# Kernel optimization log

Hardware: AMD Instinct MI355X
Metric: run time of the kernel (lower is better)

## Reference

```python
import jax, jax.numpy as jnp
import numpy as np

B, DIM, T = 8, 1024, 4096
CB, CD = 4096, 8          # codebook_size, codebook_dim
COMMIT = 0.25
EPS = 1e-12


def _weight_norm(v, g):
    # torch weight_norm over dim=0: per-output-channel norm of v
    n = jnp.sqrt(jnp.sum(v * v, axis=1, keepdims=True))
    return g[:, None] * v / n


def _l2_normalize(x):
    n = jnp.sqrt(jnp.sum(x * x, axis=1, keepdims=True))
    return x / jnp.maximum(n, EPS)


def setup_inputs() -> dict:
    key = jax.random.key(0)
    ks = jax.random.split(key, 5)
    z = jax.random.normal(ks[0], (B, DIM, T), jnp.float32)
    v_in = jax.random.normal(ks[1], (CD, DIM), jnp.float32) * 0.02   # conv1d k=1 weight (squeezed)
    g_in = jnp.sqrt(jnp.sum(v_in * v_in, axis=1))                     # weight_norm init: g = ||v||
    b_in = jnp.zeros((CD,), jnp.float32)
    codebook = jax.random.normal(ks[2], (CB, CD), jnp.float32)        # nn.Embedding default N(0,1)
    v_out = jax.random.normal(ks[3], (DIM, CD), jnp.float32) * 0.02
    g_out = jnp.sqrt(jnp.sum(v_out * v_out, axis=1))
    b_out = jnp.zeros((DIM,), jnp.float32)
    return {"z": z, "v_in": v_in, "g_in": g_in, "b_in": b_in,
            "codebook": codebook, "v_out": v_out, "g_out": g_out, "b_out": b_out}


def reference(z, v_in, g_in, b_in, codebook, v_out, g_out, b_out):
    # in_proj: weight-normed 1x1 Conv1d == per-timestep matmul
    W_in = _weight_norm(v_in, g_in)                              # [CD, DIM]
    z_e = jnp.einsum('od,bdt->bot', W_in, z) + b_in[None, :, None]  # [B, CD, T]

    # decode_latents: normalize encodings and codebook, squared-L2 distances
    enc = z_e.transpose(0, 2, 1).reshape(B * T, CD)              # (b t) d
    e_n = _l2_normalize(enc)                                     # [BT, CD]
    c_n = _l2_normalize(codebook)                                # [CB, CD]
    dist = (jnp.sum(e_n * e_n, axis=1, keepdims=True)
            - 2.0 * (e_n @ c_n.T)
            + jnp.sum(c_n * c_n, axis=1)[None, :])               # [BT, CB]
    indices = jnp.argmin(dist, axis=1).reshape(B, T)             # [B, T] int

    # decode_code: gather UN-normalized codebook, transpose to [B, CD, T]
    z_q = codebook[indices].transpose(0, 2, 1)                   # [B, CD, T]

    # training losses (per-batch), commitment + codebook
    sg = jax.lax.stop_gradient
    commitment_loss = jnp.mean((z_e - sg(z_q)) ** 2, axis=(1, 2)) * COMMIT
    codebook_loss = jnp.mean((z_q - sg(z_e)) ** 2, axis=(1, 2))
    commit_loss = commitment_loss + codebook_loss                # [B]

    # straight-through estimator
    z_q_ste = z_e + sg(z_q - z_e)                                # [B, CD, T]

    # out_proj
    W_out = _weight_norm(v_out, g_out)                           # [DIM, CD]
    out = jnp.einsum('oc,bct->bot', W_out, z_q_ste) + b_out[None, :, None]  # [B, DIM, T]
    return out, indices, commit_loss
```

## Files before the change

### kernel.cpp

```cpp
#include <hip/hip_runtime.h>

#define DIMN 1024
#define TN 4096
#define BN 8
#define CBN 4096
#define CDN 8
#define BTN (BN*TN)
#define OUT_ELEMS (BN*DIMN*TN)

typedef float fx4 __attribute__((ext_vector_type(4)));

#define WS_WINT 0
#define WS_WOUT 8192
#define WS_CN   16384
#define WS_C2   49152
#define WS_LOSS 86016
#define WS_CNT  86024
#define WS_ZEP  360448

#define LCB_F   0
#define LH_F    32768
#define LZE_F   36864
#define LEN_F   37888
#define LCAND_F 38912
#define LWO_F   0
#define LZQ_F   8192
#define LBO_F   9216

__device__ __forceinline__ float dot4(float4 a, float4 b) {
    float d = a.x * b.x;
    d = fmaf(a.y, b.y, d);
    d = fmaf(a.z, b.z, d);
    d = fmaf(a.w, b.w, d);
    return d;
}
__device__ __forceinline__ void add4(float4& a, float4 b) {
    a.x += b.x; a.y += b.y; a.z += b.z; a.w += b.w;
}

__global__ __launch_bounds__(256) void k0_prep(
    const float* __restrict__ v_in, const float* __restrict__ g_in,
    const float* __restrict__ codebook, const float* __restrict__ v_out,
    const float* __restrict__ g_out, float* __restrict__ ws) {
    __shared__ float sred[5];
    int blk = blockIdx.x, tid = threadIdx.x;
    if (blk < 8) {
        int o = blk;
        const float* v = v_in + o * DIMN;
        float4 x = *(const float4*)(v + tid * 4);
        float p = x.x * x.x + x.y * x.y + x.z * x.z + x.w * x.w;
        for (int off = 32; off >= 1; off >>= 1) p += __shfl_down(p, off, 64);
        if ((tid & 63) == 0) sred[tid >> 6] = p;
        __syncthreads();
        if (tid == 0) {
            float tot = sred[0] + sred[1] + sred[2] + sred[3];
            sred[4] = g_in[o] / sqrtf(tot);
        }
        __syncthreads();
        float s = sred[4];
        ws[WS_WINT + (tid * 4 + 0) * 8 + o] = x.x * s;
        ws[WS_WINT + (tid * 4 + 1) * 8 + o] = x.y * s;
        ws[WS_WINT + (tid * 4 + 2) * 8 + o] = x.z * s;
        ws[WS_WINT + (tid * 4 + 3) * 8 + o] = x.w * s;
    } else if (blk < 12) {
        int r = (blk - 8) * 256 + tid;
        const float* v = v_out + r * 8;
        float4 a = *(const float4*)v;
        float4 b = *(const float4*)(v + 4);
        float n2 = dot4(a, a) + dot4(b, b);
        float s = g_out[r] / sqrtf(n2);
        *(float4*)(ws + WS_WOUT + r * 8)     = make_float4(a.x*s, a.y*s, a.z*s, a.w*s);
        *(float4*)(ws + WS_WOUT + r * 8 + 4) = make_float4(b.x*s, b.y*s, b.z*s, b.w*s);
    } else if (blk < 28) {
        int j = (blk - 12) * 256 + tid;
        const float* c = codebook + j * 8;
        float4 a = *(const float4*)c;
        float4 b = *(const float4*)(c + 4);
        float n2 = dot4(a, a) + dot4(b, b);
        float inv = 1.0f / fmaxf(sqrtf(n2), 1e-12f);
        float4 na = make_float4(a.x*inv, a.y*inv, a.z*inv, a.w*inv);
        float4 nb = make_float4(b.x*inv, b.y*inv, b.z*inv, b.w*inv);
        *(float4*)(ws + WS_CN + j * 8)     = na;
        *(float4*)(ws + WS_CN + j * 8 + 4) = nb;
        ws[WS_C2 + j] = -0.5f * (dot4(na, na) + dot4(nb, nb));
    } else {
        if (tid < 9) ws[WS_LOSS + tid] = 0.0f;
    }
}

__global__ __launch_bounds__(256) void k1a_ze(
    const float* __restrict__ z, float* __restrict__ ws) {
    __shared__ float wlds[512 * 8];
    int tid = threadIdx.x, blk = blockIdx.x;
    int b = blk >> 5;
    int r = blk & 31;
    int t0 = (r >> 1) * 256;
    int dbase = (r & 1) * 512;
    #pragma unroll
    for (int i = 0; i < 4; i++) {
        int f4 = tid + i * 256;
        *(float4*)(wlds + f4 * 4) = *(const float4*)(ws + WS_WINT + dbase * 8 + f4 * 4);
    }
    __syncthreads();
    int w = tid >> 6, lane = tid & 63;
    const float* zp = z + ((size_t)(b * DIMN + dbase + w * 128)) * TN + t0 + lane * 4;
    float4 acc[8];
    #pragma unroll
    for (int c = 0; c < 8; c++) acc[c] = make_float4(0.f, 0.f, 0.f, 0.f);
    #pragma unroll 8
    for (int dd = 0; dd < 128; ++dd) {
        fx4 zr = __builtin_nontemporal_load((const fx4*)(zp + (size_t)dd * TN));
        const float* wv = wlds + (w * 128 + dd) * 8;
        #pragma unroll
        for (int c = 0; c < 8; c++) {
            float wc = wv[c];
            acc[c].x = fmaf(wc, zr.x, acc[c].x);
            acc[c].y = fmaf(wc, zr.y, acc[c].y);
            acc[c].z = fmaf(wc, zr.z, acc[c].z);
            acc[c].w = fmaf(wc, zr.w, acc[c].w);
        }
    }
    int p = (r & 1) * 4 + w;
    float* op = ws + WS_ZEP + ((size_t)p * BTN + b * TN + t0 + lane * 4) * 8;
    *(float4*)(op +  0) = make_float4(acc[0].x, acc[1].x, acc[2].x, acc[3].x);
    *(float4*)(op +  4) = make_float4(acc[4].x, acc[5].x, acc[6].x, acc[7].x);
    *(float4*)(op +  8) = make_float4(acc[0].y, acc[1].y, acc[2].y, acc[3].y);
    *(float4*)(op + 12) = make_float4(acc[4].y, acc[5].y, acc[6].y, acc[7].y);
    *(float4*)(op + 16) = make_float4(acc[0].z, acc[1].z, acc[2].z, acc[3].z);
    *(float4*)(op + 20) = make_float4(acc[4].z, acc[5].z, acc[6].z, acc[7].z);
    *(float4*)(op + 24) = make_float4(acc[0].w, acc[1].w, acc[2].w, acc[3].w);
    *(float4*)(op + 28) = make_float4(acc[4].w, acc[5].w, acc[6].w, acc[7].w);
}

__global__ __launch_bounds__(256, 1) void k_fused(
    const float* __restrict__ b_in, const float* __restrict__ codebook,
    const float* __restrict__ b_out, float* __restrict__ dout,
    float* __restrict__ ws) {
    __shared__ float sp[40960];
    int tid = threadIdx.x, blk = blockIdx.x;
    int b = blk >> 5;
    int t0 = (blk & 31) * 128;

    #pragma unroll 4
    for (int i = 0; i < 36; i++) {
        int f4 = i * 256 + tid;
        *(float4*)(sp + f4 * 4) = *(const float4*)(ws + WS_CN + f4 * 4);
    }
    if (tid < 128) {
        int bt = b * TN + t0 + tid;
        float4 za = *(const float4*)(b_in);
        float4 zb = *(const float4*)(b_in + 4);
        #pragma unroll
        for (int p = 0; p < 8; p++) {
            const float* pp = ws + WS_ZEP + ((size_t)p * BTN + bt) * 8;
            add4(za, *(const float4*)(pp));
            add4(zb, *(const float4*)(pp + 4));
        }
        *(float4*)(sp + LZE_F + tid * 8)     = za;
        *(float4*)(sp + LZE_F + tid * 8 + 4) = zb;
        float inv = 1.0f / fmaxf(sqrtf(dot4(za, za) + dot4(zb, zb)), 1e-12f);
        *(float4*)(sp + LEN_F + tid * 8)     = make_float4(za.x*inv, za.y*inv, za.z*inv, za.w*inv);
        *(float4*)(sp + LEN_F + tid * 8 + 4) = make_float4(zb.x*inv, zb.y*inv, zb.z*inv, zb.w*inv);
    }
    __syncthreads();

    int chunk = tid >> 5, tq = tid & 31;
    float e[4][8];
    #pragma unroll
    for (int tt = 0; tt < 4; tt++) {
        float4 a = *(const float4*)(sp + LEN_F + (tq * 4 + tt) * 8);
        float4 c = *(const float4*)(sp + LEN_F + (tq * 4 + tt) * 8 + 4);
        e[tt][0] = a.x; e[tt][1] = a.y; e[tt][2] = a.z; e[tt][3] = a.w;
        e[tt][4] = c.x; e[tt][5] = c.y; e[tt][6] = c.z; e[tt][7] = c.w;
    }
    float bs[4]; int bi[4];
    #pragma unroll
    for (int tt = 0; tt < 4; tt++) { bs[tt] = -3.4e38f; bi[tt] = 0; }
    const float* cb = sp + chunk * 512 * 8;
    const float* hp = sp + LH_F + chunk * 512;
    #pragma unroll 4
    for (int j = 0; j < 512; ++j) {
        float4 ca = *(const float4*)(cb + j * 8);
        float4 cc = *(const float4*)(cb + j * 8 + 4);
        float hh = hp[j];
        #pragma unroll
        for (int tt = 0; tt < 4; tt++) {
            float s = fmaf(e[tt][0], ca.x, hh);
            s = fmaf(e[tt][1], ca.y, s); s = fmaf(e[tt][2], ca.z, s); s = fmaf(e[tt][3], ca.w, s);
            s = fmaf(e[tt][4], cc.x, s); s = fmaf(e[tt][5], cc.y, s);
            s = fmaf(e[tt][6], cc.z, s); s = fmaf(e[tt][7], cc.w, s);
            if (s > bs[tt]) { bs[tt] = s; bi[tt] = j; }
        }
    }
    #pragma unroll
    for (int tt = 0; tt < 4; tt++) {
        *(float2*)(sp + LCAND_F + (chunk * 128 + tq * 4 + tt) * 2) =
            make_float2(bs[tt], __int_as_float(chunk * 512 + bi[tt]));
    }
    __syncthreads();

    if (tid < 128) {
        float2 c0 = *(const float2*)(sp + LCAND_F + tid * 2);
        float best = c0.x; int idx = __float_as_int(c0.y);
        #pragma unroll
        for (int ch = 1; ch < 8; ch++) {
            float2 cc = *(const float2*)(sp + LCAND_F + (ch * 128 + tid) * 2);
            if (cc.x > best) { best = cc.x; idx = __float_as_int(cc.y); }
        }
        dout[(size_t)OUT_ELEMS + b * TN + t0 + tid] = (float)idx;
        const float* cq = codebook + (size_t)idx * 8;
        float4 qa = *(const float4*)cq, qb = *(const float4*)(cq + 4);
        sp[LZQ_F + 0*128 + tid] = qa.x; sp[LZQ_F + 1*128 + tid] = qa.y;
        sp[LZQ_F + 2*128 + tid] = qa.z; sp[LZQ_F + 3*128 + tid] = qa.w;
        sp[LZQ_F + 4*128 + tid] = qb.x; sp[LZQ_F + 5*128 + tid] = qb.y;
        sp[LZQ_F + 6*128 + tid] = qb.z; sp[LZQ_F + 7*128 + tid] = qb.w;
        float4 za = *(const float4*)(sp + LZE_F + tid * 8);
        float4 zb = *(const float4*)(sp + LZE_F + tid * 8 + 4);
        float4 da = make_float4(za.x-qa.x, za.y-qa.y, za.z-qa.z, za.w-qa.w);
        float4 db = make_float4(zb.x-qb.x, zb.y-qb.y, zb.z-qb.z, zb.w-qb.w);
        float l = dot4(da, da) + dot4(db, db);
        for (int off = 32; off >= 1; off >>= 1) l += __shfl_down(l, off, 64);
        if ((tid & 63) == 0) atomicAdd(ws + WS_LOSS + b, l);
    } else {
        int k = tid - 128;
        #pragma unroll 4
        for (int i = 0; i < 16; i++) {
            int f4 = i * 128 + k;
            *(float4*)(sp + LWO_F + f4 * 4) = *(const float4*)(ws + WS_WOUT + f4 * 4);
        }
        #pragma unroll
        for (int i = 0; i < 2; i++) {
            int f4 = i * 128 + k;
            *(float4*)(sp + LBO_F + f4 * 4) = *(const float4*)(b_out + f4 * 4);
        }
    }
    __syncthreads();

    int t4 = tid & 31, osub = tid >> 5;
    int tqf = t4 * 4;
    float4 zr[8];
    #pragma unroll
    for (int c = 0; c < 8; c++) zr[c] = *(const float4*)(sp + LZQ_F + c * 128 + tqf);
    size_t obase = ((size_t)(b * DIMN)) * TN + (size_t)(t0 + tqf);
    for (int k = 0; k < 128; k++) {
        int o = osub * 128 + k;
        float4 wa = *(const float4*)(sp + LWO_F + o * 8);
        float4 wb = *(const float4*)(sp + LWO_F + o * 8 + 4);
        float bo = sp[LBO_F + o];
        float4 acc = make_float4(bo, bo, bo, bo);
        float wc[8] = {wa.x, wa.y, wa.z, wa.w, wb.x, wb.y, wb.z, wb.w};
        #pragma unroll
        for (int c = 0; c < 8; c++) {
            acc.x = fmaf(wc[c], zr[c].x, acc.x);
            acc.y = fmaf(wc[c], zr[c].y, acc.y);
            acc.z = fmaf(wc[c], zr[c].z, acc.z);
            acc.w = fmaf(wc[c], zr[c].w, acc.w);
        }
        acc.x = fminf(fmaxf(acc.x, -8.f), 8.f);
        acc.y = fminf(fmaxf(acc.y, -8.f), 8.f);
        acc.z = fminf(fmaxf(acc.z, -8.f), 8.f);
        acc.w = fminf(fmaxf(acc.w, -8.f), 8.f);
        fx4 st; st.x = acc.x; st.y = acc.y; st.z = acc.z; st.w = acc.w;
        __builtin_nontemporal_store(st, (fx4*)(dout + obase + (size_t)o * TN));
    }

    if (tid == 0) {
        __threadfence();
        unsigned int old = atomicAdd((unsigned int*)(ws + WS_CNT), 1u);
        if (old == 255u) {
            #pragma unroll
            for (int i = 0; i < 8; i++) {
                float v = atomicAdd(ws + WS_LOSS + i, 0.0f);
                dout[(size_t)OUT_ELEMS + BTN + i] = v * (1.25f / 32768.0f);
            }
        }
    }
}

extern "C" void kernel_launch(void* const* d_in, const int* in_sizes, int n_in,
                              void* d_out, int out_size, void* d_ws, size_t ws_size,
                              hipStream_t stream) {
    (void)in_sizes; (void)n_in; (void)out_size; (void)ws_size;
    const float* z        = (const float*)d_in[0];
    const float* v_in     = (const float*)d_in[1];
    const float* g_in     = (const float*)d_in[2];
    const float* b_in     = (const float*)d_in[3];
    const float* codebook = (const float*)d_in[4];
    const float* v_out    = (const float*)d_in[5];
    const float* g_out    = (const float*)d_in[6];
    const float* b_out    = (const float*)d_in[7];
    float* out            = (float*)d_out;
    float* ws             = (float*)d_ws;

    hipLaunchKernelGGL(k0_prep, dim3(29), dim3(256), 0, stream,
                       v_in, g_in, codebook, v_out, g_out, ws);
    hipLaunchKernelGGL(k1a_ze, dim3(256), dim3(256), 0, stream, z, ws);
    hipLaunchKernelGGL(k_fused, dim3(256), dim3(256), 0, stream,
                       b_in, codebook, b_out, out, ws);
}
```

Before: 321.7 us.

## Stream codebook through small LDS chunks and halve per-block tile for occupancy

The fused search/out-projection kernel now processes 64 timesteps per block across 512 blocks instead of 128 across 256. The normalized codebook and its norm term are streamed into a small LDS buffer in four chunks of 1024 entries rather than loaded whole. This cuts LDS use from about 160KB to about 47KB so two blocks can share a CU. The out_proj weights and bias are stored padded to reduce bank conflicts, and the argmin merge gains a lowest-index tie-break. The cost is extra barriers and reloading of the codebook chunks per block.

```diff
diff --git a/kernel.cpp b/kernel.cpp
--- a/kernel.cpp
+++ b/kernel.cpp
@@ -18,14 +18,13 @@
 #define WS_CNT  86024
 #define WS_ZEP  360448
 
-#define LCB_F   0
-#define LH_F    32768
-#define LZE_F   36864
-#define LEN_F   37888
-#define LCAND_F 38912
-#define LWO_F   0
-#define LZQ_F   8192
-#define LBO_F   9216
+#define LH_F    8192
+#define LBO_F   8256
+#define LZE_F   9296
+#define LEN_F   9808
+#define LCAND_F 10320
+#define LZQ_F   11344
+#define LDS_TOT 11856
 
 __device__ __forceinline__ float dot4(float4 a, float4 b) {
     float d = a.x * b.x;
@@ -132,21 +131,16 @@
     *(float4*)(op + 28) = make_float4(acc[4].w, acc[5].w, acc[6].w, acc[7].w);
 }
 
-__global__ __launch_bounds__(256, 1) void k_fused(
+__global__ __launch_bounds__(256, 2) void k_so(
     const float* __restrict__ b_in, const float* __restrict__ codebook,
     const float* __restrict__ b_out, float* __restrict__ dout,
     float* __restrict__ ws) {
-    __shared__ float sp[40960];
+    __shared__ float sp[LDS_TOT];
     int tid = threadIdx.x, blk = blockIdx.x;
-    int b = blk >> 5;
-    int t0 = (blk & 31) * 128;
-
-    #pragma unroll 4
-    for (int i = 0; i < 36; i++) {
-        int f4 = i * 256 + tid;
-        *(float4*)(sp + f4 * 4) = *(const float4*)(ws + WS_CN + f4 * 4);
-    }
-    if (tid < 128) {
+    int b = blk >> 6;
+    int t0 = (blk & 63) * 64;
+
+    if (tid < 64) {
         int bt = b * TN + t0 + tid;
         float4 za = *(const float4*)(b_in);
         float4 zb = *(const float4*)(b_in + 4);
@@ -161,92 +155,138 @@
         float inv = 1.0f / fmaxf(sqrtf(dot4(za, za) + dot4(zb, zb)), 1e-12f);
         *(float4*)(sp + LEN_F + tid * 8)     = make_float4(za.x*inv, za.y*inv, za.z*inv, za.w*inv);
         *(float4*)(sp + LEN_F + tid * 8 + 4) = make_float4(zb.x*inv, zb.y*inv, zb.z*inv, zb.w*inv);
+    } else {
+        int i = tid - 64;
+        #pragma unroll
+        for (int r = 0; r < 12; r++) {
+            int f4 = r * 192 + i;
+            if (f4 < 2048) {
+                *(float4*)(sp + f4 * 4) = *(const float4*)(ws + WS_CN + f4 * 4);
+            } else {
+                int g = f4 - 2048;
+                *(float4*)(sp + LH_F + g * 4) = *(const float4*)(ws + WS_C2 + g * 4);
+            }
+        }
     }
     __syncthreads();
 
-    int chunk = tid >> 5, tq = tid & 31;
-    float e[4][8];
-    #pragma unroll
-    for (int tt = 0; tt < 4; tt++) {
-        float4 a = *(const float4*)(sp + LEN_F + (tq * 4 + tt) * 8);
-        float4 c = *(const float4*)(sp + LEN_F + (tq * 4 + tt) * 8 + 4);
-        e[tt][0] = a.x; e[tt][1] = a.y; e[tt][2] = a.z; e[tt][3] = a.w;
-        e[tt][4] = c.x; e[tt][5] = c.y; e[tt][6] = c.z; e[tt][7] = c.w;
-    }
-    float bs[4]; int bi[4];
-    #pragma unroll
-    for (int tt = 0; tt < 4; tt++) { bs[tt] = -3.4e38f; bi[tt] = 0; }
-    const float* cb = sp + chunk * 512 * 8;
-    const float* hp = sp + LH_F + chunk * 512;
-    #pragma unroll 4
-    for (int j = 0; j < 512; ++j) {
-        float4 ca = *(const float4*)(cb + j * 8);
-        float4 cc = *(const float4*)(cb + j * 8 + 4);
-        float hh = hp[j];
-        #pragma unroll
-        for (int tt = 0; tt < 4; tt++) {
-            float s = fmaf(e[tt][0], ca.x, hh);
-            s = fmaf(e[tt][1], ca.y, s); s = fmaf(e[tt][2], ca.z, s); s = fmaf(e[tt][3], ca.w, s);
-            s = fmaf(e[tt][4], cc.x, s); s = fmaf(e[tt][5], cc.y, s);
-            s = fmaf(e[tt][6], cc.z, s); s = fmaf(e[tt][7], cc.w, s);
-            if (s > bs[tt]) { bs[tt] = s; bi[tt] = j; }
-        }
-    }
-    #pragma unroll
-    for (int tt = 0; tt < 4; tt++) {
-        *(float2*)(sp + LCAND_F + (chunk * 128 + tq * 4 + tt) * 2) =
-            make_float2(bs[tt], __int_as_float(chunk * 512 + bi[tt]));
-    }
+    int t2 = tid & 31, q = tid >> 5;
+    int ta = t2 * 2, tb = ta + 1;
+    float ea[8], eb[8];
+    {
+        float4 a0 = *(const float4*)(sp + LEN_F + ta * 8);
+        float4 a1 = *(const float4*)(sp + LEN_F + ta * 8 + 4);
+        float4 b0 = *(const float4*)(sp + LEN_F + tb * 8);
+        float4 b1 = *(const float4*)(sp + LEN_F + tb * 8 + 4);
+        ea[0]=a0.x; ea[1]=a0.y; ea[2]=a0.z; ea[3]=a0.w;
+        ea[4]=a1.x; ea[5]=a1.y; ea[6]=a1.z; ea[7]=a1.w;
+        eb[0]=b0.x; eb[1]=b0.y; eb[2]=b0.z; eb[3]=b0.w;
+        eb[4]=b1.x; eb[5]=b1.y; eb[6]=b1.z; eb[7]=b1.w;
+    }
+
+    float bs0 = -3.4e38f, bs1 = -3.4e38f;
+    int bj0 = 0, bj1 = 0;
+    const float* cbp = sp + q * 128 * 8;
+    const float* hp  = sp + LH_F + q * 128;
+
+    for (int c = 0; c < 4; c++) {
+        if (c > 0) {
+            #pragma unroll
+            for (int r = 0; r < 9; r++) {
+                int f4 = r * 256 + tid;
+                if (f4 < 2048) {
+                    *(float4*)(sp + f4 * 4) = *(const float4*)(ws + WS_CN + (size_t)c * 8192 + f4 * 4);
+                } else {
+                    int g = f4 - 2048;
+                    *(float4*)(sp + LH_F + g * 4) = *(const float4*)(ws + WS_C2 + c * 1024 + g * 4);
+                }
+            }
+            __syncthreads();
+        }
+        int jg = c * 1024 + q * 128;
+        #pragma unroll 4
+        for (int j = 0; j < 128; ++j) {
+            float4 ca = *(const float4*)(cbp + j * 8);
+            float4 cc = *(const float4*)(cbp + j * 8 + 4);
+            float hh = hp[j];
+            float s0 = fmaf(ea[0], ca.x, hh);
+            s0 = fmaf(ea[1], ca.y, s0); s0 = fmaf(ea[2], ca.z, s0); s0 = fmaf(ea[3], ca.w, s0);
+            s0 = fmaf(ea[4], cc.x, s0); s0 = fmaf(ea[5], cc.y, s0);
+            s0 = fmaf(ea[6], cc.z, s0); s0 = fmaf(ea[7], cc.w, s0);
+            float s1 = fmaf(eb[0], ca.x, hh);
+            s1 = fmaf(eb[1], ca.y, s1); s1 = fmaf(eb[2], ca.z, s1); s1 = fmaf(eb[3], ca.w, s1);
+            s1 = fmaf(eb[4], cc.x, s1); s1 = fmaf(eb[5], cc.y, s1);
+            s1 = fmaf(eb[6], cc.z, s1); s1 = fmaf(eb[7], cc.w, s1);
+            if (s0 > bs0) { bs0 = s0; bj0 = jg + j; }
+            if (s1 > bs1) { bs1 = s1; bj1 = jg + j; }
+        }
+        __syncthreads();
+    }
+
+    *(float4*)(sp + LCAND_F + (q * 64 + ta) * 2) =
+        make_float4(bs0, __int_as_float(bj0), bs1, __int_as_float(bj1));
     __syncthreads();
 
-    if (tid < 128) {
-        float2 c0 = *(const float2*)(sp + LCAND_F + tid * 2);
+    if (tid < 64) {
+        int t = tid;
+        float2 c0 = *(const float2*)(sp + LCAND_F + t * 2);
         float best = c0.x; int idx = __float_as_int(c0.y);
         #pragma unroll
-        for (int ch = 1; ch < 8; ch++) {
-            float2 cc = *(const float2*)(sp + LCAND_F + (ch * 128 + tid) * 2);
-            if (cc.x > best) { best = cc.x; idx = __float_as_int(cc.y); }
-        }
-        dout[(size_t)OUT_ELEMS + b * TN + t0 + tid] = (float)idx;
+        for (int q2 = 1; q2 < 8; q2++) {
+            float2 cq = *(const float2*)(sp + LCAND_F + (q2 * 64 + t) * 2);
+            int j2 = __float_as_int(cq.y);
+            if (cq.x > best || (cq.x == best && j2 < idx)) { best = cq.x; idx = j2; }
+        }
+        dout[(size_t)OUT_ELEMS + b * TN + t0 + t] = (float)idx;
         const float* cq = codebook + (size_t)idx * 8;
         float4 qa = *(const float4*)cq, qb = *(const float4*)(cq + 4);
-        sp[LZQ_F + 0*128 + tid] = qa.x; sp[LZQ_F + 1*128 + tid] = qa.y;
-        sp[LZQ_F + 2*128 + tid] = qa.z; sp[LZQ_F + 3*128 + tid] = qa.w;
-        sp[LZQ_F + 4*128 + tid] = qb.x; sp[LZQ_F + 5*128 + tid] = qb.y;
-        sp[LZQ_F + 6*128 + tid] = qb.z; sp[LZQ_F + 7*128 + tid] = qb.w;
-        float4 za = *(const float4*)(sp + LZE_F + tid * 8);
-        float4 zb = *(const float4*)(sp + LZE_F + tid * 8 + 4);
+        sp[LZQ_F + 0*64 + t] = qa.x; sp[LZQ_F + 1*64 + t] = qa.y;
+        sp[LZQ_F + 2*64 + t] = qa.z; sp[LZQ_F + 3*64 + t] = qa.w;
+        sp[LZQ_F + 4*64 + t] = qb.x; sp[LZQ_F + 5*64 + t] = qb.y;
+        sp[LZQ_F + 6*64 + t] = qb.z; sp[LZQ_F + 7*64 + t] = qb.w;
+        float4 za = *(const float4*)(sp + LZE_F + t * 8);
+        float4 zb = *(const float4*)(sp + LZE_F + t * 8 + 4);
         float4 da = make_float4(za.x-qa.x, za.y-qa.y, za.z-qa.z, za.w-qa.w);
         float4 db = make_float4(zb.x-qb.x, zb.y-qb.y, zb.z-qb.z, zb.w-qb.w);
         float l = dot4(da, da) + dot4(db, db);
         for (int off = 32; off >= 1; off >>= 1) l += __shfl_down(l, off, 64);
-        if ((tid & 63) == 0) atomicAdd(ws + WS_LOSS + b, l);
+        if (t == 0) atomicAdd(ws + WS_LOSS + b, l);
     } else {
-        int k = tid - 128;
-        #pragma unroll 4
-        for (int i = 0; i < 16; i++) {
-            int f4 = i * 128 + k;
-            *(float4*)(sp + LWO_F + f4 * 4) = *(const float4*)(ws + WS_WOUT + f4 * 4);
-        }
-        #pragma unroll
-        for (int i = 0; i < 2; i++) {
-            int f4 = i * 128 + k;
-            *(float4*)(sp + LBO_F + f4 * 4) = *(const float4*)(b_out + f4 * 4);
+        int i = tid - 64;
+        #pragma unroll
+        for (int r = 0; r < 11; r++) {
+            int f4 = r * 192 + i;
+            if (f4 < 2048) {
+                float4 v = *(const float4*)(ws + WS_WOUT + f4 * 4);
+                *(float4*)(sp + f4 * 4 + 4 * (f4 >> 7)) = v;
+            }
+        }
+        #pragma unroll
+        for (int r = 0; r < 2; r++) {
+            int f = r * 192 + i;
+            if (f < 256) {
+                float4 v = *(const float4*)(b_out + f * 4);
+                int sk = f >> 4;
+                sp[LBO_F + f * 4 + sk + 0] = v.x;
+                sp[LBO_F + f * 4 + sk + 1] = v.y;
+                sp[LBO_F + f * 4 + sk + 2] = v.z;
+                sp[LBO_F + f * 4 + sk + 3] = v.w;
+            }
         }
     }
     __syncthreads();
 
-    int t4 = tid & 31, osub = tid >> 5;
-    int tqf = t4 * 4;
+    int t4 = tid & 15, og = tid >> 4;
     float4 zr[8];
     #pragma unroll
-    for (int c = 0; c < 8; c++) zr[c] = *(const float4*)(sp + LZQ_F + c * 128 + tqf);
-    size_t obase = ((size_t)(b * DIMN)) * TN + (size_t)(t0 + tqf);
-    for (int k = 0; k < 128; k++) {
-        int o = osub * 128 + k;
-        float4 wa = *(const float4*)(sp + LWO_F + o * 8);
-        float4 wb = *(const float4*)(sp + LWO_F + o * 8 + 4);
-        float bo = sp[LBO_F + o];
+    for (int c = 0; c < 8; c++) zr[c] = *(const float4*)(sp + LZQ_F + c * 64 + t4 * 4);
+    size_t obase = ((size_t)(b * DIMN + og * 64)) * TN + (size_t)(t0 + t4 * 4);
+    for (int k = 0; k < 64; k++) {
+        int o = og * 64 + k;
+        const float* wrow = sp + o * 8 + 4 * og;
+        float4 wa = *(const float4*)(wrow);
+        float4 wb = *(const float4*)(wrow + 4);
+        float bo = sp[LBO_F + o + og];
         float4 acc = make_float4(bo, bo, bo, bo);
         float wc[8] = {wa.x, wa.y, wa.z, wa.w, wb.x, wb.y, wb.z, wb.w};
         #pragma unroll
@@ -261,13 +301,13 @@
         acc.z = fminf(fmaxf(acc.z, -8.f), 8.f);
         acc.w = fminf(fmaxf(acc.w, -8.f), 8.f);
         fx4 st; st.x = acc.x; st.y = acc.y; st.z = acc.z; st.w = acc.w;
-        __builtin_nontemporal_store(st, (fx4*)(dout + obase + (size_t)o * TN));
+        __builtin_nontemporal_store(st, (fx4*)(dout + obase + (size_t)k * TN));
     }
 
     if (tid == 0) {
         __threadfence();
         unsigned int old = atomicAdd((unsigned int*)(ws + WS_CNT), 1u);
-        if (old == 255u) {
+        if (old == 511u) {
             #pragma unroll
             for (int i = 0; i < 8; i++) {
                 float v = atomicAdd(ws + WS_LOSS + i, 0.0f);
@@ -295,6 +335,6 @@
     hipLaunchKernelGGL(k0_prep, dim3(29), dim3(256), 0, stream,
                        v_in, g_in, codebook, v_out, g_out, ws);
     hipLaunchKernelGGL(k1a_ze, dim3(256), dim3(256), 0, stream, z, ws);
-    hipLaunchKernelGGL(k_fused, dim3(256), dim3(256), 0, stream,
+    hipLaunchKernelGGL(k_so, dim3(512), dim3(256), 0, stream,
                        b_in, codebook, b_out, out, ws);
 }
```

After: 306.1 us. -4.8%, faster.
